# Optimization experiments

Measured on AMD Instinct MI355X. Metric: run time of the kernel, lower is better.

Reference implementation:

```python
import jax, jax.numpy as jnp
import numpy as np

EPS = 1e-12


def _l2normalize(x):
    # F.normalize(x, p=2, dim=1): x / max(||x||_2, eps)
    n = jnp.sqrt(jnp.sum(x * x, axis=1, keepdims=True))
    return x / jnp.maximum(n, EPS)


def setup_inputs() -> dict:
    key = jax.random.key(0)
    ks = jax.random.split(key, 20)
    B, J, SD, OD = 16384, 10, 8, 4
    H = 10 * (SD + OD)            # 120 gru hidden
    OH = 4 * SD * OD              # 128 output-head hidden
    IN = SD + OD                  # 12
    s = 0.1
    return {
        "y_t": jax.random.normal(ks[0], (B, OD), jnp.float32),
        "x_filtered_prev": jax.random.normal(ks[1], (B, SD), jnp.float32),
        "delta_x_prev": jax.random.normal(ks[2], (B, SD), jnp.float32),
        "h_prev_ensemble": jax.random.normal(ks[3], (J, B, H), jnp.float32),
        "F_mat": jnp.eye(SD) + 0.05 * jax.random.normal(ks[4], (SD, SD), jnp.float32),
        "H_mat": jax.random.normal(ks[5], (OD, SD), jnp.float32) * 0.3,
        "W_fc1": jax.random.normal(ks[6], (H, IN), jnp.float32) * s,
        "b_fc1": jax.random.normal(ks[7], (H,), jnp.float32) * s,
        "W_ih": jax.random.normal(ks[8], (3 * H, H), jnp.float32) * s,
        "W_hh": jax.random.normal(ks[9], (3 * H, H), jnp.float32) * s,
        "b_ih": jax.random.normal(ks[10], (3 * H,), jnp.float32) * s,
        "b_hh": jax.random.normal(ks[11], (3 * H,), jnp.float32) * s,
        "W_fc2": jax.random.normal(ks[12], (OH, H), jnp.float32) * s,
        "b_fc2": jax.random.normal(ks[13], (OH,), jnp.float32) * s,
        "W_fc3": jax.random.normal(ks[14], (SD * OD, OH), jnp.float32) * s,
        "b_fc3": jax.random.normal(ks[15], (SD * OD,), jnp.float32) * s,
        "p_logit1": jnp.array([0.5], jnp.float32),   # sigmoid ~ 0.62 in [0.5,0.8)
        "p_logit2": jnp.array([0.8], jnp.float32),
        "u1": jax.random.uniform(ks[16], (J, B, H), jnp.float32),
        "u2": jax.random.uniform(ks[17], (J, B, OH), jnp.float32),
    }


def reference(y_t, x_filtered_prev, delta_x_prev, h_prev_ensemble,
              F_mat, H_mat, W_fc1, b_fc1, W_ih, W_hh, b_ih, b_hh,
              W_fc2, b_fc2, W_fc3, b_fc3, p_logit1, p_logit2, u1, u2):
    B = y_t.shape[0]
    SD = x_filtered_prev.shape[1]
    OD = y_t.shape[1]
    Hd = W_ih.shape[1]

    # --- prediction (vectorized version of the per-sample f/h loops) ---
    x_predicted = x_filtered_prev @ F_mat.T          # [B, SD]
    y_predicted = x_predicted @ H_mat.T              # [B, OD]
    innovation = y_t - y_predicted                   # [B, OD]

    # --- DNN input, shared across J (dropout masks differ per sample) ---
    nn_input = jnp.concatenate([_l2normalize(delta_x_prev),
                                _l2normalize(innovation)], axis=1)  # [B, IN]

    p1 = jax.nn.sigmoid(p_logit1[0])
    p2 = jax.nn.sigmoid(p_logit2[0])
    mask1 = (u1 >= p1).astype(jnp.float32) / (1.0 - p1)   # [J,B,Hd]
    mask2 = (u2 >= p2).astype(jnp.float32) / (1.0 - p2)   # [J,B,OH]

    # input FC + ReLU, then MC-dropout per ensemble sample -> [J,B,Hd]
    a1 = jax.nn.relu(nn_input @ W_fc1.T + b_fc1)[None, :, :] * mask1

    # --- single-layer GRU cell, batched over (J, B) ---
    gx = a1 @ W_ih.T + b_ih                     # [J,B,3Hd]
    gh = h_prev_ensemble @ W_hh.T + b_hh        # [J,B,3Hd]
    gx_r, gx_z, gx_n = jnp.split(gx, 3, axis=-1)
    gh_r, gh_z, gh_n = jnp.split(gh, 3, axis=-1)
    r = jax.nn.sigmoid(gx_r + gh_r)
    z = jax.nn.sigmoid(gx_z + gh_z)
    n = jnp.tanh(gx_n + r * gh_n)
    h_new_ensemble = (1.0 - z) * n + z * h_prev_ensemble   # [J,B,Hd]

    # output head + MC-dropout -> Kalman gain per sample
    a2 = jax.nn.relu(h_new_ensemble @ W_fc2.T + b_fc2) * mask2   # [J,B,OH]
    K_vec = a2 @ W_fc3.T + b_fc3                                  # [J,B,SD*OD]
    K = K_vec.reshape(K_vec.shape[0], B, SD, OD)

    correction = jnp.einsum('jbso,bo->jbs', K, innovation)       # [J,B,SD]
    x_filtered_ensemble = x_predicted[None, :, :] + correction   # [J,B,SD]

    x_filtered_final = x_filtered_ensemble.mean(axis=0)          # [B,SD]
    diff = x_filtered_ensemble - x_filtered_final[None]
    P_filtered_final = jnp.einsum('jbs,jbt->bst', diff, diff) / diff.shape[0]

    # concrete-dropout style regularizer (identical per sample -> mean == value)
    def _ent(p):
        return p * jnp.log(p) + (1.0 - p) * jnp.log1p(-p)
    avg_regularization = (jnp.sum(W_fc1 ** 2) / (1.0 - p1) + _ent(p1)
                          + jnp.sum(W_fc2 ** 2) / (1.0 - p2) + _ent(p2))

    return x_filtered_final, P_filtered_final, avg_regularization
```

## Files before the change

### kernel.cpp

```cpp
#include <hip/hip_runtime.h>
#include <hip/hip_bf16.h>
#include <math.h>

#define B_SIZE 16384
#define J_ENS  10

#define U_WB1   0
#define U_WB2   131072
#define U_WB3   147456
#define U_A1S   152576
#define F_GB    75776
#define F_XPRED 1059328
#define F_INNOV 1190400
#define F_CORR  1255936

typedef __attribute__((ext_vector_type(8))) short s16x8;
typedef __attribute__((ext_vector_type(4))) float f32x4;

__device__ __forceinline__ float sigm(float x) { return 1.f / (1.f + expf(-x)); }
__device__ __forceinline__ float fsigm(float x) { return __builtin_amdgcn_rcpf(1.f + __expf(-x)); }
__device__ __forceinline__ float ftanh(float x) {
    float e = __expf(2.f * x);
    return 1.f - 2.f * __builtin_amdgcn_rcpf(e + 1.f);
}
__device__ __forceinline__ unsigned short f2bf(float x) {
    __hip_bfloat16 h = __float2bfloat16(x);
    return __builtin_bit_cast(unsigned short, h);
}

__global__ void prep_kernel(const float* __restrict__ Wih, const float* __restrict__ Whh,
                            const float* __restrict__ bih, const float* __restrict__ bhh,
                            const float* __restrict__ Wfc2, const float* __restrict__ Wfc3,
                            float* __restrict__ ws) {
    unsigned short* wsu = (unsigned short*)ws;
    int idx = blockIdx.x * 256 + threadIdx.x;
    if (idx < 131072) {
        int n = idx >> 8, k = idx & 255;
        int cb = n >> 7, nn = n & 127;
        float v = 0.f;
        if (nn < 120) {
            if (cb == 0)      v = (k < 120) ? Wih[nn * 120 + k]         : ((k < 240) ? Whh[nn * 120 + (k - 120)] : 0.f);
            else if (cb == 1) v = (k < 120) ? Wih[(120 + nn) * 120 + k] : ((k < 240) ? Whh[(120 + nn) * 120 + (k - 120)] : 0.f);
            else if (cb == 2) v = (k < 120) ? Wih[(240 + nn) * 120 + k] : 0.f;
            else              v = (k >= 120 && k < 240) ? Whh[(240 + nn) * 120 + (k - 120)] : 0.f;
        }
        wsu[U_WB1 + idx] = f2bf(v);
    } else if (idx < 147456) {
        int i2 = idx - 131072; int o = i2 >> 7, k = i2 & 127;
        wsu[U_WB2 + i2] = f2bf((k < 120) ? Wfc2[o * 120 + k] : 0.f);
    } else if (idx < 151552) {
        int i3 = idx - 147456;
        wsu[U_WB3 + i3] = f2bf(Wfc3[i3]);
    } else if (idx < 152064) {
        int i4 = idx - 151552; int g = i4 >> 7, n = i4 & 127;
        float v = 0.f;
        if (n < 120) {
            if (g == 0)      v = bih[n] + bhh[n];
            else if (g == 1) v = bih[120 + n] + bhh[120 + n];
            else if (g == 2) v = bih[240 + n];
            else             v = bhh[240 + n];
        }
        ws[F_GB + i4] = v;
    }
}

__global__ void pre_kernel(const float* __restrict__ y_t, const float* __restrict__ xprev,
                           const float* __restrict__ dxprev, const float* __restrict__ F,
                           const float* __restrict__ Hm, const float* __restrict__ W1,
                           const float* __restrict__ b1, const float* __restrict__ pl1,
                           float* __restrict__ ws) {
    int b = blockIdx.x * blockDim.x + threadIdx.x;
    if (b >= B_SIZE) return;
    unsigned short* wsu = (unsigned short*)ws;
    float p1 = sigm(pl1[0]);
    float i1 = 1.f / (1.f - p1);
    float xf[8], dx[8], xp[8];
#pragma unroll
    for (int t = 0; t < 8; ++t) { xf[t] = xprev[b * 8 + t]; dx[t] = dxprev[b * 8 + t]; }
#pragma unroll
    for (int s = 0; s < 8; ++s) {
        float a = 0.f;
#pragma unroll
        for (int t = 0; t < 8; ++t) a = fmaf(F[s * 8 + t], xf[t], a);
        xp[s] = a;
    }
    float inn[4];
#pragma unroll
    for (int o = 0; o < 4; ++o) {
        float a = 0.f;
#pragma unroll
        for (int s = 0; s < 8; ++s) a = fmaf(Hm[o * 8 + s], xp[s], a);
        inn[o] = y_t[b * 4 + o] - a;
    }
    float nd = 0.f, ni = 0.f;
#pragma unroll
    for (int s = 0; s < 8; ++s) nd = fmaf(dx[s], dx[s], nd);
#pragma unroll
    for (int o = 0; o < 4; ++o) ni = fmaf(inn[o], inn[o], ni);
    nd = fmaxf(sqrtf(nd), 1e-12f);
    ni = fmaxf(sqrtf(ni), 1e-12f);
    float nn[12];
#pragma unroll
    for (int s = 0; s < 8; ++s) nn[s] = dx[s] / nd;
#pragma unroll
    for (int o = 0; o < 4; ++o) nn[8 + o] = inn[o] / ni;
    for (int n = 0; n < 120; ++n) {
        float a = b1[n];
#pragma unroll
        for (int i = 0; i < 12; ++i) a = fmaf(W1[n * 12 + i], nn[i], a);
        wsu[U_A1S + b * 120 + n] = f2bf(fmaxf(a, 0.f) * i1);
    }
#pragma unroll
    for (int s = 0; s < 8; ++s) ws[F_XPRED + b * 8 + s] = xp[s];
#pragma unroll
    for (int o = 0; o < 4; ++o) ws[F_INNOV + b * 4 + o] = inn[o];
}

__launch_bounds__(256, 2)
__global__ void main_kernel(const float* __restrict__ hprev, const float* __restrict__ u1,
                            const float* __restrict__ u2, const float* __restrict__ b2,
                            const float* __restrict__ b3, const float* __restrict__ pl1,
                            const float* __restrict__ pl2, float* __restrict__ ws) {
    __shared__ unsigned short Xl[64 * 264];
    __shared__ unsigned short Hn[64 * 136];
    __shared__ unsigned short A2l[64 * 136];
    __shared__ float Kvl[64 * 40];

    const unsigned short* WB1p = (const unsigned short*)ws + U_WB1;
    const unsigned short* WB2p = (const unsigned short*)ws + U_WB2;
    const unsigned short* WB3p = (const unsigned short*)ws + U_WB3;
    const unsigned short* a1s  = (const unsigned short*)ws + U_A1S;
    const float* GB = ws + F_GB;

    const int t  = threadIdx.x;
    const int r0 = blockIdx.x * 64;
    const int b0 = r0 & (B_SIZE - 1);

    const float p1 = sigm(pl1[0]);
    const float p2 = sigm(pl2[0]);
    const float i2 = 1.f / (1.f - p2);

    for (int idx = t; idx < 1920; idx += 256) {
        int m = idx / 30, q = (idx % 30) * 4;
        float4 uu = *(const float4*)&u1[(size_t)(r0 + m) * 120 + q];
        ushort4 aa = *(const ushort4*)&a1s[(b0 + m) * 120 + q];
        ushort4 xv;
        xv.x = (uu.x >= p1) ? aa.x : (unsigned short)0;
        xv.y = (uu.y >= p1) ? aa.y : (unsigned short)0;
        xv.z = (uu.z >= p1) ? aa.z : (unsigned short)0;
        xv.w = (uu.w >= p1) ? aa.w : (unsigned short)0;
        *(ushort4*)&Xl[m * 264 + q] = xv;
        float4 hh = *(const float4*)&hprev[(size_t)(r0 + m) * 120 + q];
        ushort4 hv;
        hv.x = f2bf(hh.x); hv.y = f2bf(hh.y); hv.z = f2bf(hh.z); hv.w = f2bf(hh.w);
        *(ushort4*)&Xl[m * 264 + 120 + q] = hv;
    }
    for (int idx = t; idx < 512; idx += 256) {
        int m = idx >> 3, c = 240 + ((idx & 7) << 1);
        ushort2 z; z.x = 0; z.y = 0;
        *(ushort2*)&Xl[m * 264 + c] = z;
    }
    {
        int m = t >> 2, c = 120 + ((t & 3) << 1);
        ushort2 z; z.x = 0; z.y = 0;
        *(ushort2*)&Hn[m * 136 + c] = z;
    }
    __syncthreads();

    const int wv = t >> 6;
    const int ln = t & 63;
    const int lr = ln & 15;
    const int kg = (ln >> 4) * 8;
    const int rbase = (ln >> 4) * 4;

    f32x4 acc[32];
#pragma unroll
    for (int i = 0; i < 32; ++i) acc[i] = (f32x4){0.f, 0.f, 0.f, 0.f};
#pragma unroll
    for (int ks = 0; ks < 8; ++ks) {
        s16x8 af[4];
#pragma unroll
        for (int mf = 0; mf < 4; ++mf)
            af[mf] = *(const s16x8*)&Xl[(mf * 16 + lr) * 264 + ks * 32 + kg];
#pragma unroll
        for (int g = 0; g < 4; ++g) {
#pragma unroll
            for (int cf = 0; cf < 2; ++cf) {
                s16x8 bf = *(const s16x8*)&WB1p[(size_t)(g * 128 + wv * 32 + cf * 16 + lr) * 256 + ks * 32 + kg];
#pragma unroll
                for (int mf = 0; mf < 4; ++mf)
                    acc[mf * 8 + g * 2 + cf] =
                        __builtin_amdgcn_mfma_f32_16x16x32_bf16(af[mf], bf, acc[mf * 8 + g * 2 + cf], 0, 0, 0);
            }
        }
    }

#pragma unroll
    for (int cf = 0; cf < 2; ++cf) {
        int c = wv * 32 + cf * 16 + lr;
        if (c < 120) {
            float br = GB[c], bz = GB[128 + c], bx = GB[256 + c], bg = GB[384 + c];
#pragma unroll
            for (int mf = 0; mf < 4; ++mf) {
                f32x4 rA = acc[mf * 8 + 0 + cf];
                f32x4 zA = acc[mf * 8 + 2 + cf];
                f32x4 xA = acc[mf * 8 + 4 + cf];
                f32x4 gA = acc[mf * 8 + 6 + cf];
#pragma unroll
                for (int rr = 0; rr < 4; ++rr) {
                    int row = mf * 16 + rbase + rr;
                    float hp = hprev[(size_t)(r0 + row) * 120 + c];
                    float r = fsigm(rA[rr] + br);
                    float z = fsigm(zA[rr] + bz);
                    float n = ftanh(xA[rr] + bx + r * (gA[rr] + bg));
                    Hn[row * 136 + c] = f2bf((1.f - z) * n + z * hp);
                }
            }
        }
    }
    __syncthreads();

    f32x4 acc2[8];
#pragma unroll
    for (int i = 0; i < 8; ++i) acc2[i] = (f32x4){0.f, 0.f, 0.f, 0.f};
#pragma unroll
    for (int ks = 0; ks < 4; ++ks) {
        s16x8 af[4];
#pragma unroll
        for (int mf = 0; mf < 4; ++mf)
            af[mf] = *(const s16x8*)&Hn[(mf * 16 + lr) * 136 + ks * 32 + kg];
#pragma unroll
        for (int cf = 0; cf < 2; ++cf) {
            s16x8 bf = *(const s16x8*)&WB2p[(wv * 32 + cf * 16 + lr) * 128 + ks * 32 + kg];
#pragma unroll
            for (int mf = 0; mf < 4; ++mf)
                acc2[mf * 2 + cf] =
                    __builtin_amdgcn_mfma_f32_16x16x32_bf16(af[mf], bf, acc2[mf * 2 + cf], 0, 0, 0);
        }
    }
#pragma unroll
    for (int cf = 0; cf < 2; ++cf) {
        int c = wv * 32 + cf * 16 + lr;
        float bb = b2[c];
#pragma unroll
        for (int mf = 0; mf < 4; ++mf) {
#pragma unroll
            for (int rr = 0; rr < 4; ++rr) {
                int row = mf * 16 + rbase + rr;
                float uu = u2[(size_t)(r0 + row) * 128 + c];
                float v = fmaxf(acc2[mf * 2 + cf][rr] + bb, 0.f);
                v = (uu >= p2) ? v * i2 : 0.f;
                A2l[row * 136 + c] = f2bf(v);
            }
        }
    }
    __syncthreads();

    {
        const int m0 = wv * 16;
        f32x4 a3[2];
#pragma unroll
        for (int i = 0; i < 2; ++i) a3[i] = (f32x4){0.f, 0.f, 0.f, 0.f};
#pragma unroll
        for (int ks = 0; ks < 4; ++ks) {
            s16x8 a = *(const s16x8*)&A2l[(m0 + lr) * 136 + ks * 32 + kg];
#pragma unroll
            for (int nf = 0; nf < 2; ++nf) {
                s16x8 bf = *(const s16x8*)&WB3p[(nf * 16 + lr) * 128 + ks * 32 + kg];
                a3[nf] = __builtin_amdgcn_mfma_f32_16x16x32_bf16(a, bf, a3[nf], 0, 0, 0);
            }
        }
#pragma unroll
        for (int nf = 0; nf < 2; ++nf) {
            int c = nf * 16 + lr;
            float bb = b3[c];
#pragma unroll
            for (int rr = 0; rr < 4; ++rr) {
                int row = m0 + rbase + rr;
                Kvl[row * 40 + c] = a3[nf][rr] + bb;
            }
        }
    }
    __syncthreads();

    for (int idx = t; idx < 512; idx += 256) {
        int m = idx >> 3, s = idx & 7;
        float4 iv = *(const float4*)&ws[F_INNOV + (b0 + m) * 4];
        const float* kv = &Kvl[m * 40 + s * 4];
        ws[F_CORR + (size_t)(r0 + m) * 8 + s] =
            fmaf(kv[3], iv.w, fmaf(kv[2], iv.z, fmaf(kv[1], iv.y, kv[0] * iv.x)));
    }
}

__global__ void reduce_kernel(const float* __restrict__ ws, float* __restrict__ out) {
    int b = blockIdx.x * 256 + threadIdx.x;
    if (b >= B_SIZE) return;
    const float* corr  = ws + F_CORR;
    const float* xpred = ws + F_XPRED;
    float S[8];
    float SS[64];
#pragma unroll
    for (int s = 0; s < 8; ++s) S[s] = 0.f;
#pragma unroll
    for (int q = 0; q < 64; ++q) SS[q] = 0.f;
    for (int j = 0; j < J_ENS; ++j) {
        float c[8];
        float4 c0 = *(const float4*)&corr[(size_t)(j * B_SIZE + b) * 8];
        float4 c1 = *(const float4*)&corr[(size_t)(j * B_SIZE + b) * 8 + 4];
        c[0] = c0.x; c[1] = c0.y; c[2] = c0.z; c[3] = c0.w;
        c[4] = c1.x; c[5] = c1.y; c[6] = c1.z; c[7] = c1.w;
#pragma unroll
        for (int s = 0; s < 8; ++s) S[s] += c[s];
#pragma unroll
        for (int s = 0; s < 8; ++s)
#pragma unroll
            for (int tt = 0; tt < 8; ++tt) SS[s * 8 + tt] = fmaf(c[s], c[tt], SS[s * 8 + tt]);
    }
    const float invJ = 1.f / (float)J_ENS;
    float mc[8];
#pragma unroll
    for (int s = 0; s < 8; ++s) {
        mc[s] = S[s] * invJ;
        out[b * 8 + s] = xpred[b * 8 + s] + mc[s];
    }
#pragma unroll
    for (int s = 0; s < 8; ++s)
#pragma unroll
        for (int tt = 0; tt < 8; ++tt)
            out[131072 + b * 64 + s * 8 + tt] = SS[s * 8 + tt] * invJ - mc[s] * mc[tt];
}

__global__ void reg_kernel(const float* __restrict__ W1, const float* __restrict__ W2,
                           const float* __restrict__ pl1, const float* __restrict__ pl2,
                           float* __restrict__ out) {
    __shared__ float red[256];
    int t = threadIdx.x;
    float s1 = 0.f, s2 = 0.f;
    for (int i = t; i < 1440; i += 256)  { float v = W1[i]; s1 = fmaf(v, v, s1); }
    for (int i = t; i < 15360; i += 256) { float v = W2[i]; s2 = fmaf(v, v, s2); }
    red[t] = s1; __syncthreads();
    for (int s = 128; s > 0; s >>= 1) { if (t < s) red[t] += red[t + s]; __syncthreads(); }
    float r1 = red[0]; __syncthreads();
    red[t] = s2; __syncthreads();
    for (int s = 128; s > 0; s >>= 1) { if (t < s) red[t] += red[t + s]; __syncthreads(); }
    if (t == 0) {
        float p1 = sigm(pl1[0]), p2 = sigm(pl2[0]);
        float e1 = p1 * logf(p1) + (1.f - p1) * logf(1.f - p1);
        float e2 = p2 * logf(p2) + (1.f - p2) * logf(1.f - p2);
        out[1179648] = r1 / (1.f - p1) + e1 + red[0] / (1.f - p2) + e2;
    }
}

extern "C" void kernel_launch(void* const* d_in, const int* in_sizes, int n_in,
                              void* d_out, int out_size, void* d_ws, size_t ws_size,
                              hipStream_t stream) {
    const float* y_t   = (const float*)d_in[0];
    const float* xfp   = (const float*)d_in[1];
    const float* dxp   = (const float*)d_in[2];
    const float* hprev = (const float*)d_in[3];
    const float* F     = (const float*)d_in[4];
    const float* Hm    = (const float*)d_in[5];
    const float* W1    = (const float*)d_in[6];
    const float* b1    = (const float*)d_in[7];
    const float* Wih   = (const float*)d_in[8];
    const float* Whh   = (const float*)d_in[9];
    const float* bih   = (const float*)d_in[10];
    const float* bhh   = (const float*)d_in[11];
    const float* W2    = (const float*)d_in[12];
    const float* b2    = (const float*)d_in[13];
    const float* W3    = (const float*)d_in[14];
    const float* b3    = (const float*)d_in[15];
    const float* pl1   = (const float*)d_in[16];
    const float* pl2   = (const float*)d_in[17];
    const float* u1    = (const float*)d_in[18];
    const float* u2    = (const float*)d_in[19];
    float* out = (float*)d_out;
    float* ws  = (float*)d_ws;

    prep_kernel<<<dim3(594), dim3(256), 0, stream>>>(Wih, Whh, bih, bhh, W2, W3, ws);
    pre_kernel<<<dim3(64), dim3(256), 0, stream>>>(y_t, xfp, dxp, F, Hm, W1, b1, pl1, ws);
    main_kernel<<<dim3(2560), dim3(256), 0, stream>>>(hprev, u1, u2, b2, b3, pl1, pl2, ws);
    reduce_kernel<<<dim3(64), dim3(256), 0, stream>>>(ws, out);
    reg_kernel<<<dim3(1), dim3(256), 0, stream>>>(W1, W2, pl1, pl2, out);
}
```

Before: 415.6 us.

## Widen main kernel to 512 threads, alias shared memory, parallelize pre and reduce

The main fused GRU/MLP kernel now uses 8 waves per 64-row tile, so each wave computes half as many output columns with half the accumulator registers. Shared memory is aliased (X and A2 buffers overlap) so more blocks can be resident, and the launch bounds target higher occupancy. The pre kernel now stages W1 in LDS and spreads the fc1 output over all threads. The reduce kernel runs more, smaller blocks, and the regularizer kernel is folded into an extra prep block to remove one launch. The risks are more barrier overhead per tile and the buffer aliasing relying on correct synchronization ordering.

```diff
diff --git a/kernel.cpp b/kernel.cpp
--- a/kernel.cpp
+++ b/kernel.cpp
@@ -31,7 +31,28 @@
 __global__ void prep_kernel(const float* __restrict__ Wih, const float* __restrict__ Whh,
                             const float* __restrict__ bih, const float* __restrict__ bhh,
                             const float* __restrict__ Wfc2, const float* __restrict__ Wfc3,
+                            const float* __restrict__ W1, const float* __restrict__ pl1,
+                            const float* __restrict__ pl2, float* __restrict__ out,
                             float* __restrict__ ws) {
+    if (blockIdx.x == 594) {
+        __shared__ float red[256];
+        int t = threadIdx.x;
+        float s1 = 0.f, s2 = 0.f;
+        for (int i = t; i < 1440; i += 256)  { float v = W1[i];  s1 = fmaf(v, v, s1); }
+        for (int i = t; i < 15360; i += 256) { float v = Wfc2[i]; s2 = fmaf(v, v, s2); }
+        red[t] = s1; __syncthreads();
+        for (int s = 128; s > 0; s >>= 1) { if (t < s) red[t] += red[t + s]; __syncthreads(); }
+        float r1 = red[0]; __syncthreads();
+        red[t] = s2; __syncthreads();
+        for (int s = 128; s > 0; s >>= 1) { if (t < s) red[t] += red[t + s]; __syncthreads(); }
+        if (t == 0) {
+            float p1 = sigm(pl1[0]), p2 = sigm(pl2[0]);
+            float e1 = p1 * logf(p1) + (1.f - p1) * logf(1.f - p1);
+            float e2 = p2 * logf(p2) + (1.f - p2) * logf(1.f - p2);
+            out[1179648] = r1 / (1.f - p1) + e1 + red[0] / (1.f - p2) + e2;
+        }
+        return;
+    }
     unsigned short* wsu = (unsigned short*)ws;
     int idx = blockIdx.x * 256 + threadIdx.x;
     if (idx < 131072) {
@@ -69,62 +90,75 @@
                            const float* __restrict__ Hm, const float* __restrict__ W1,
                            const float* __restrict__ b1, const float* __restrict__ pl1,
                            float* __restrict__ ws) {
-    int b = blockIdx.x * blockDim.x + threadIdx.x;
-    if (b >= B_SIZE) return;
+    __shared__ float nnl[64][12];
+    __shared__ float W1l[1440];
+    __shared__ float b1l[120];
     unsigned short* wsu = (unsigned short*)ws;
-    float p1 = sigm(pl1[0]);
-    float i1 = 1.f / (1.f - p1);
-    float xf[8], dx[8], xp[8];
-#pragma unroll
-    for (int t = 0; t < 8; ++t) { xf[t] = xprev[b * 8 + t]; dx[t] = dxprev[b * 8 + t]; }
-#pragma unroll
-    for (int s = 0; s < 8; ++s) {
-        float a = 0.f;
-#pragma unroll
-        for (int t = 0; t < 8; ++t) a = fmaf(F[s * 8 + t], xf[t], a);
-        xp[s] = a;
-    }
-    float inn[4];
-#pragma unroll
-    for (int o = 0; o < 4; ++o) {
-        float a = 0.f;
-#pragma unroll
-        for (int s = 0; s < 8; ++s) a = fmaf(Hm[o * 8 + s], xp[s], a);
-        inn[o] = y_t[b * 4 + o] - a;
-    }
-    float nd = 0.f, ni = 0.f;
-#pragma unroll
-    for (int s = 0; s < 8; ++s) nd = fmaf(dx[s], dx[s], nd);
-#pragma unroll
-    for (int o = 0; o < 4; ++o) ni = fmaf(inn[o], inn[o], ni);
-    nd = fmaxf(sqrtf(nd), 1e-12f);
-    ni = fmaxf(sqrtf(ni), 1e-12f);
-    float nn[12];
-#pragma unroll
-    for (int s = 0; s < 8; ++s) nn[s] = dx[s] / nd;
-#pragma unroll
-    for (int o = 0; o < 4; ++o) nn[8 + o] = inn[o] / ni;
-    for (int n = 0; n < 120; ++n) {
-        float a = b1[n];
-#pragma unroll
-        for (int i = 0; i < 12; ++i) a = fmaf(W1[n * 12 + i], nn[i], a);
-        wsu[U_A1S + b * 120 + n] = f2bf(fmaxf(a, 0.f) * i1);
-    }
-#pragma unroll
-    for (int s = 0; s < 8; ++s) ws[F_XPRED + b * 8 + s] = xp[s];
-#pragma unroll
-    for (int o = 0; o < 4; ++o) ws[F_INNOV + b * 4 + o] = inn[o];
-}
-
-__launch_bounds__(256, 2)
+    const int t  = threadIdx.x;
+    const int b0 = blockIdx.x * 64;
+    const float p1 = sigm(pl1[0]);
+    const float i1 = 1.f / (1.f - p1);
+
+    for (int i = t; i < 1440; i += 256) W1l[i] = W1[i];
+    if (t < 120) b1l[t] = b1[t];
+
+    if (t < 64) {
+        int b = b0 + t;
+        float xf[8], dx[8], xp[8];
+#pragma unroll
+        for (int s = 0; s < 8; ++s) { xf[s] = xprev[b * 8 + s]; dx[s] = dxprev[b * 8 + s]; }
+#pragma unroll
+        for (int s = 0; s < 8; ++s) {
+            float a = 0.f;
+#pragma unroll
+            for (int q = 0; q < 8; ++q) a = fmaf(F[s * 8 + q], xf[q], a);
+            xp[s] = a;
+        }
+        float inn[4];
+#pragma unroll
+        for (int o = 0; o < 4; ++o) {
+            float a = 0.f;
+#pragma unroll
+            for (int s = 0; s < 8; ++s) a = fmaf(Hm[o * 8 + s], xp[s], a);
+            inn[o] = y_t[b * 4 + o] - a;
+        }
+        float nd = 0.f, ni = 0.f;
+#pragma unroll
+        for (int s = 0; s < 8; ++s) nd = fmaf(dx[s], dx[s], nd);
+#pragma unroll
+        for (int o = 0; o < 4; ++o) ni = fmaf(inn[o], inn[o], ni);
+        nd = fmaxf(sqrtf(nd), 1e-12f);
+        ni = fmaxf(sqrtf(ni), 1e-12f);
+#pragma unroll
+        for (int s = 0; s < 8; ++s) nnl[t][s] = dx[s] / nd;
+#pragma unroll
+        for (int o = 0; o < 4; ++o) nnl[t][8 + o] = inn[o] / ni;
+#pragma unroll
+        for (int s = 0; s < 8; ++s) ws[F_XPRED + b * 8 + s] = xp[s];
+#pragma unroll
+        for (int o = 0; o < 4; ++o) ws[F_INNOV + b * 4 + o] = inn[o];
+    }
+    __syncthreads();
+
+    for (int idx = t; idx < 7680; idx += 256) {
+        int m = idx / 120, n = idx % 120;
+        float a = b1l[n];
+#pragma unroll
+        for (int i = 0; i < 12; ++i) a = fmaf(W1l[n * 12 + i], nnl[m][i], a);
+        wsu[U_A1S + (size_t)(b0 + m) * 120 + n] = f2bf(fmaxf(a, 0.f) * i1);
+    }
+}
+
+__launch_bounds__(512, 6)
 __global__ void main_kernel(const float* __restrict__ hprev, const float* __restrict__ u1,
                             const float* __restrict__ u2, const float* __restrict__ b2,
                             const float* __restrict__ b3, const float* __restrict__ pl1,
                             const float* __restrict__ pl2, float* __restrict__ ws) {
-    __shared__ unsigned short Xl[64 * 264];
-    __shared__ unsigned short Hn[64 * 136];
-    __shared__ unsigned short A2l[64 * 136];
-    __shared__ float Kvl[64 * 40];
+    __shared__ unsigned char smem[51200];
+    unsigned short* Xl  = (unsigned short*)smem;
+    unsigned short* A2l = (unsigned short*)smem;
+    float*          Kvl = (float*)(smem + 17408);
+    unsigned short* Hn  = (unsigned short*)(smem + 33792);
 
     const unsigned short* WB1p = (const unsigned short*)ws + U_WB1;
     const unsigned short* WB2p = (const unsigned short*)ws + U_WB2;
@@ -140,7 +174,7 @@
     const float p2 = sigm(pl2[0]);
     const float i2 = 1.f / (1.f - p2);
 
-    for (int idx = t; idx < 1920; idx += 256) {
+    for (int idx = t; idx < 1920; idx += 512) {
         int m = idx / 30, q = (idx % 30) * 4;
         float4 uu = *(const float4*)&u1[(size_t)(r0 + m) * 120 + q];
         ushort4 aa = *(const ushort4*)&a1s[(b0 + m) * 120 + q];
@@ -155,12 +189,12 @@
         hv.x = f2bf(hh.x); hv.y = f2bf(hh.y); hv.z = f2bf(hh.z); hv.w = f2bf(hh.w);
         *(ushort4*)&Xl[m * 264 + 120 + q] = hv;
     }
-    for (int idx = t; idx < 512; idx += 256) {
-        int m = idx >> 3, c = 240 + ((idx & 7) << 1);
+    {
+        int m = t >> 3, c = 240 + ((t & 7) << 1);
         ushort2 z; z.x = 0; z.y = 0;
         *(ushort2*)&Xl[m * 264 + c] = z;
     }
-    {
+    if (t < 256) {
         int m = t >> 2, c = 120 + ((t & 3) << 1);
         ushort2 z; z.x = 0; z.y = 0;
         *(ushort2*)&Hn[m * 136 + c] = z;
@@ -173,9 +207,9 @@
     const int kg = (ln >> 4) * 8;
     const int rbase = (ln >> 4) * 4;
 
-    f32x4 acc[32];
-#pragma unroll
-    for (int i = 0; i < 32; ++i) acc[i] = (f32x4){0.f, 0.f, 0.f, 0.f};
+    f32x4 acc[16];
+#pragma unroll
+    for (int i = 0; i < 16; ++i) acc[i] = (f32x4){0.f, 0.f, 0.f, 0.f};
 #pragma unroll
     for (int ks = 0; ks < 8; ++ks) {
         s16x8 af[4];
@@ -184,28 +218,24 @@
             af[mf] = *(const s16x8*)&Xl[(mf * 16 + lr) * 264 + ks * 32 + kg];
 #pragma unroll
         for (int g = 0; g < 4; ++g) {
-#pragma unroll
-            for (int cf = 0; cf < 2; ++cf) {
-                s16x8 bf = *(const s16x8*)&WB1p[(size_t)(g * 128 + wv * 32 + cf * 16 + lr) * 256 + ks * 32 + kg];
-#pragma unroll
-                for (int mf = 0; mf < 4; ++mf)
-                    acc[mf * 8 + g * 2 + cf] =
-                        __builtin_amdgcn_mfma_f32_16x16x32_bf16(af[mf], bf, acc[mf * 8 + g * 2 + cf], 0, 0, 0);
-            }
-        }
-    }
-
-#pragma unroll
-    for (int cf = 0; cf < 2; ++cf) {
-        int c = wv * 32 + cf * 16 + lr;
+            s16x8 bf = *(const s16x8*)&WB1p[(size_t)(g * 128 + wv * 16 + lr) * 256 + ks * 32 + kg];
+#pragma unroll
+            for (int mf = 0; mf < 4; ++mf)
+                acc[mf * 4 + g] =
+                    __builtin_amdgcn_mfma_f32_16x16x32_bf16(af[mf], bf, acc[mf * 4 + g], 0, 0, 0);
+        }
+    }
+
+    {
+        int c = wv * 16 + lr;
         if (c < 120) {
             float br = GB[c], bz = GB[128 + c], bx = GB[256 + c], bg = GB[384 + c];
 #pragma unroll
             for (int mf = 0; mf < 4; ++mf) {
-                f32x4 rA = acc[mf * 8 + 0 + cf];
-                f32x4 zA = acc[mf * 8 + 2 + cf];
-                f32x4 xA = acc[mf * 8 + 4 + cf];
-                f32x4 gA = acc[mf * 8 + 6 + cf];
+                f32x4 rA = acc[mf * 4 + 0];
+                f32x4 zA = acc[mf * 4 + 1];
+                f32x4 xA = acc[mf * 4 + 2];
+                f32x4 gA = acc[mf * 4 + 3];
 #pragma unroll
                 for (int rr = 0; rr < 4; ++rr) {
                     int row = mf * 16 + rbase + rr;
@@ -220,27 +250,22 @@
     }
     __syncthreads();
 
-    f32x4 acc2[8];
-#pragma unroll
-    for (int i = 0; i < 8; ++i) acc2[i] = (f32x4){0.f, 0.f, 0.f, 0.f};
+    f32x4 acc2[4];
+#pragma unroll
+    for (int i = 0; i < 4; ++i) acc2[i] = (f32x4){0.f, 0.f, 0.f, 0.f};
 #pragma unroll
     for (int ks = 0; ks < 4; ++ks) {
         s16x8 af[4];
 #pragma unroll
         for (int mf = 0; mf < 4; ++mf)
             af[mf] = *(const s16x8*)&Hn[(mf * 16 + lr) * 136 + ks * 32 + kg];
-#pragma unroll
-        for (int cf = 0; cf < 2; ++cf) {
-            s16x8 bf = *(const s16x8*)&WB2p[(wv * 32 + cf * 16 + lr) * 128 + ks * 32 + kg];
-#pragma unroll
-            for (int mf = 0; mf < 4; ++mf)
-                acc2[mf * 2 + cf] =
-                    __builtin_amdgcn_mfma_f32_16x16x32_bf16(af[mf], bf, acc2[mf * 2 + cf], 0, 0, 0);
-        }
-    }
-#pragma unroll
-    for (int cf = 0; cf < 2; ++cf) {
-        int c = wv * 32 + cf * 16 + lr;
+        s16x8 bf = *(const s16x8*)&WB2p[(wv * 16 + lr) * 128 + ks * 32 + kg];
+#pragma unroll
+        for (int mf = 0; mf < 4; ++mf)
+            acc2[mf] = __builtin_amdgcn_mfma_f32_16x16x32_bf16(af[mf], bf, acc2[mf], 0, 0, 0);
+    }
+    {
+        int c = wv * 16 + lr;
         float bb = b2[c];
 #pragma unroll
         for (int mf = 0; mf < 4; ++mf) {
@@ -248,7 +273,7 @@
             for (int rr = 0; rr < 4; ++rr) {
                 int row = mf * 16 + rbase + rr;
                 float uu = u2[(size_t)(r0 + row) * 128 + c];
-                float v = fmaxf(acc2[mf * 2 + cf][rr] + bb, 0.f);
+                float v = fmaxf(acc2[mf][rr] + bb, 0.f);
                 v = (uu >= p2) ? v * i2 : 0.f;
                 A2l[row * 136 + c] = f2bf(v);
             }
@@ -257,34 +282,27 @@
     __syncthreads();
 
     {
-        const int m0 = wv * 16;
-        f32x4 a3[2];
-#pragma unroll
-        for (int i = 0; i < 2; ++i) a3[i] = (f32x4){0.f, 0.f, 0.f, 0.f};
+        const int m0 = (wv & 3) * 16;
+        const int cg = (wv >> 2) * 16;
+        f32x4 a3 = (f32x4){0.f, 0.f, 0.f, 0.f};
 #pragma unroll
         for (int ks = 0; ks < 4; ++ks) {
             s16x8 a = *(const s16x8*)&A2l[(m0 + lr) * 136 + ks * 32 + kg];
-#pragma unroll
-            for (int nf = 0; nf < 2; ++nf) {
-                s16x8 bf = *(const s16x8*)&WB3p[(nf * 16 + lr) * 128 + ks * 32 + kg];
-                a3[nf] = __builtin_amdgcn_mfma_f32_16x16x32_bf16(a, bf, a3[nf], 0, 0, 0);
-            }
-        }
-#pragma unroll
-        for (int nf = 0; nf < 2; ++nf) {
-            int c = nf * 16 + lr;
-            float bb = b3[c];
-#pragma unroll
-            for (int rr = 0; rr < 4; ++rr) {
-                int row = m0 + rbase + rr;
-                Kvl[row * 40 + c] = a3[nf][rr] + bb;
-            }
-        }
-    }
-    __syncthreads();
-
-    for (int idx = t; idx < 512; idx += 256) {
-        int m = idx >> 3, s = idx & 7;
+            s16x8 bf = *(const s16x8*)&WB3p[(cg + lr) * 128 + ks * 32 + kg];
+            a3 = __builtin_amdgcn_mfma_f32_16x16x32_bf16(a, bf, a3, 0, 0, 0);
+        }
+        int c = cg + lr;
+        float bb = b3[c];
+#pragma unroll
+        for (int rr = 0; rr < 4; ++rr) {
+            int row = m0 + rbase + rr;
+            Kvl[row * 40 + c] = a3[rr] + bb;
+        }
+    }
+    __syncthreads();
+
+    {
+        int m = t >> 3, s = t & 7;
         float4 iv = *(const float4*)&ws[F_INNOV + (b0 + m) * 4];
         const float* kv = &Kvl[m * 40 + s * 4];
         ws[F_CORR + (size_t)(r0 + m) * 8 + s] =
@@ -293,7 +311,7 @@
 }
 
 __global__ void reduce_kernel(const float* __restrict__ ws, float* __restrict__ out) {
-    int b = blockIdx.x * 256 + threadIdx.x;
+    int b = blockIdx.x * 64 + threadIdx.x;
     if (b >= B_SIZE) return;
     const float* corr  = ws + F_CORR;
     const float* xpred = ws + F_XPRED;
@@ -328,27 +346,6 @@
 #pragma unroll
         for (int tt = 0; tt < 8; ++tt)
             out[131072 + b * 64 + s * 8 + tt] = SS[s * 8 + tt] * invJ - mc[s] * mc[tt];
-}
-
-__global__ void reg_kernel(const float* __restrict__ W1, const float* __restrict__ W2,
-                           const float* __restrict__ pl1, const float* __restrict__ pl2,
-                           float* __restrict__ out) {
-    __shared__ float red[256];
-    int t = threadIdx.x;
-    float s1 = 0.f, s2 = 0.f;
-    for (int i = t; i < 1440; i += 256)  { float v = W1[i]; s1 = fmaf(v, v, s1); }
-    for (int i = t; i < 15360; i += 256) { float v = W2[i]; s2 = fmaf(v, v, s2); }
-    red[t] = s1; __syncthreads();
-    for (int s = 128; s > 0; s >>= 1) { if (t < s) red[t] += red[t + s]; __syncthreads(); }
-    float r1 = red[0]; __syncthreads();
-    red[t] = s2; __syncthreads();
-    for (int s = 128; s > 0; s >>= 1) { if (t < s) red[t] += red[t + s]; __syncthreads(); }
-    if (t == 0) {
-        float p1 = sigm(pl1[0]), p2 = sigm(pl2[0]);
-        float e1 = p1 * logf(p1) + (1.f - p1) * logf(1.f - p1);
-        float e2 = p2 * logf(p2) + (1.f - p2) * logf(1.f - p2);
-        out[1179648] = r1 / (1.f - p1) + e1 + red[0] / (1.f - p2) + e2;
-    }
 }
 
 extern "C" void kernel_launch(void* const* d_in, const int* in_sizes, int n_in,
@@ -377,9 +374,8 @@
     float* out = (float*)d_out;
     float* ws  = (float*)d_ws;
 
-    prep_kernel<<<dim3(594), dim3(256), 0, stream>>>(Wih, Whh, bih, bhh, W2, W3, ws);
-    pre_kernel<<<dim3(64), dim3(256), 0, stream>>>(y_t, xfp, dxp, F, Hm, W1, b1, pl1, ws);
-    main_kernel<<<dim3(2560), dim3(256), 0, stream>>>(hprev, u1, u2, b2, b3, pl1, pl2, ws);
-    reduce_kernel<<<dim3(64), dim3(256), 0, stream>>>(ws, out);
-    reg_kernel<<<dim3(1), dim3(256), 0, stream>>>(W1, W2, pl1, pl2, out);
-}
+    prep_kernel<<<dim3(595), dim3(256), 0, stream>>>(Wih, Whh, bih, bhh, W2, W3, W1, pl1, pl2, out, ws);
+    pre_kernel<<<dim3(256), dim3(256), 0, stream>>>(y_t, xfp, dxp, F, Hm, W1, b1, pl1, ws);
+    main_kernel<<<dim3(2560), dim3(512), 0, stream>>>(hprev, u1, u2, b2, b3, pl1, pl2, ws);
+    reduce_kernel<<<dim3(256), dim3(64), 0, stream>>>(ws, out);
+}
```

New measurement: 782.6 us. 88.3% more time.
